# Kernel tuning notes

Hardware: AMD Instinct MI355X
Metric: run time of the kernel (lower is better)

The kernel has to match this reference:

```python
import jax, jax.numpy as jnp
import numpy as np

B, S, H, NH = 2, 2048, 1024, 16
HD = H // NH
ROTARY_DIM = 64
EPS = 1e-5
MINUS_INF = -10000.0


def _apply_rotary(q, k, rotary_dim):
    # q, k: [B, S, NH, HD]; GPT-NeoX style rotate_half on first rotary_dim dims
    pos = jnp.arange(S, dtype=jnp.float32)
    inv_freq = 1.0 / (10000.0 ** (jnp.arange(0, rotary_dim, 2, dtype=jnp.float32) / rotary_dim))
    freqs = pos[:, None] * inv_freq[None, :]                      # [S, rd/2]
    cos = jnp.concatenate([jnp.cos(freqs)] * 2, -1)[None, :, None, :]  # [1,S,1,rd]
    sin = jnp.concatenate([jnp.sin(freqs)] * 2, -1)[None, :, None, :]

    def rot(t):
        t_rot, t_pass = t[..., :rotary_dim], t[..., rotary_dim:]
        t1, t2 = jnp.split(t_rot, 2, axis=-1)
        rotated = jnp.concatenate([-t2, t1], axis=-1)
        return jnp.concatenate([t_rot * cos + rotated * sin, t_pass], axis=-1)

    return rot(q), rot(k)


def setup_inputs() -> dict:
    key = jax.random.key(0)
    ks = jax.random.split(key, 6)
    w_scale = 0.02
    return {
        "x": jax.random.normal(ks[0], (B, S, H), jnp.float32),
        "input_mask": jnp.ones((B, S), jnp.int32),
        "norm_w": jnp.ones((H,), jnp.float32),
        "norm_b": jnp.zeros((H,), jnp.float32),
        "attn_qkvw": jax.random.normal(ks[1], (H, 3 * H), jnp.float32) * w_scale,
        "attn_qkvb": jax.random.normal(ks[2], (3 * H,), jnp.float32) * w_scale,
        "attn_ow": jax.random.normal(ks[3], (H, H), jnp.float32) * w_scale,
        "attn_ob": jax.random.normal(ks[4], (H,), jnp.float32) * w_scale,
    }


def reference(x, input_mask, norm_w, norm_b, attn_qkvw, attn_qkvb, attn_ow, attn_ob):
    # pre-layernorm (qkv_gemm path with config.pre_layer_norm)
    mu = x.mean(-1, keepdims=True)
    var = x.var(-1, keepdims=True)
    xn = (x - mu) * jax.lax.rsqrt(var + EPS) * norm_w + norm_b

    # fused QKV projection
    qkv = xn @ attn_qkvw + attn_qkvb                       # [B,S,3H]
    q, k, v = jnp.split(qkv, 3, axis=-1)
    q = q.reshape(B, S, NH, HD)
    k = k.reshape(B, S, NH, HD)
    v = v.reshape(B, S, NH, HD)

    # rotary embedding on q,k
    q, k = _apply_rotary(q, k, ROTARY_DIM)

    # scaled scores + mask bias (1 - mask) * -10000 + triangular masking
    scale = 1.0 / np.sqrt(HD).astype(np.float32)
    scores = jnp.einsum("bqhd,bkhd->bhqk", q, k) * scale   # [B,NH,S,S]
    mask_bias = (1.0 - input_mask.astype(scores.dtype)) * MINUS_INF
    scores = scores + mask_bias[:, None, None, :]
    causal = jnp.tril(jnp.ones((S, S), bool))
    scores = jnp.where(causal[None, None], scores, MINUS_INF)

    probs = jax.nn.softmax(scores, axis=-1)
    ctx = jnp.einsum("bhqk,bkhd->bqhd", probs, v).reshape(B, S, H)

    # output projection (vector_matmul + bias)
    return ctx @ attn_ow + attn_ob
```

## Files before the change

kernel.cpp:

```cpp
#include <hip/hip_runtime.h>
#include <hip/hip_bf16.h>

#define B_  2
#define S_  2048
#define H_  1024
#define NH_ 16
#define HD_ 64
#define T_  (B_*S_)
#define H3_ (3*H_)

typedef float  floatx4 __attribute__((ext_vector_type(4)));
typedef __bf16 bf16x8  __attribute__((ext_vector_type(8)));

__device__ inline unsigned short f2bf_rn(float f) {
    union { float f; unsigned int u; } v; v.f = f;
    unsigned int u = v.u;
    u += 0x7fffu + ((u >> 16) & 1u);
    return (unsigned short)(u >> 16);
}
__device__ inline unsigned short f2bf_tr(float f) {
    union { float f; unsigned int u; } v; v.f = f;
    return (unsigned short)(v.u >> 16);
}
__device__ inline floatx4 fzero4() { floatx4 v; v[0]=0.f; v[1]=0.f; v[2]=0.f; v[3]=0.f; return v; }

__device__ inline void gload_lds16(const unsigned short* g, unsigned short* l) {
    __builtin_amdgcn_global_load_lds((const __attribute__((address_space(1))) unsigned int*)g,
                                     (__attribute__((address_space(3))) unsigned int*)l,
                                     16, 0, 0);
}

#define TLD 72
__global__ __launch_bounds__(256) void cvt_both_k(const float* __restrict__ qkvw,
                                                  const float* __restrict__ ow,
                                                  unsigned short* __restrict__ qkvwT,
                                                  unsigned short* __restrict__ owT) {
    __shared__ unsigned short Ts[64 * TLD];
    int id = blockIdx.x;
    const float* W; unsigned short* Wt; int N, nb, kb;
    if (id < 768) { W = qkvw; Wt = qkvwT; N = H3_; nb = (id % 48) * 64; kb = (id / 48) * 64; }
    else { id -= 768; W = ow; Wt = owT; N = H_; nb = (id % 16) * 64; kb = (id / 16) * 64; }
    const int K = H_;
    const int tid = threadIdx.x;
    #pragma unroll
    for (int p = 0; p < 4; p++) {
        const int krow = kb + p * 16 + (tid >> 4);
        const int ncol = (tid & 15) * 4;
        const float4 w = *reinterpret_cast<const float4*>(&W[(size_t)krow * N + nb + ncol]);
        Ts[(ncol + 0) * TLD + p * 16 + (tid >> 4)] = f2bf_rn(w.x);
        Ts[(ncol + 1) * TLD + p * 16 + (tid >> 4)] = f2bf_rn(w.y);
        Ts[(ncol + 2) * TLD + p * 16 + (tid >> 4)] = f2bf_rn(w.z);
        Ts[(ncol + 3) * TLD + p * 16 + (tid >> 4)] = f2bf_rn(w.w);
    }
    __syncthreads();
    #pragma unroll
    for (int p = 0; p < 2; p++) {
        const int n = (tid >> 3) + p * 32;
        const int k8 = (tid & 7) * 8;
        const uint4 v = *reinterpret_cast<const uint4*>(&Ts[n * TLD + k8]);
        *reinterpret_cast<uint4*>(&Wt[(size_t)(nb + n) * K + kb + k8]) = v;
    }
}

__global__ __launch_bounds__(256) void layernorm_k(const float* __restrict__ x,
                                                   const float* __restrict__ w,
                                                   const float* __restrict__ b,
                                                   unsigned short* __restrict__ xn) {
    const int t   = blockIdx.x;
    const int tid = threadIdx.x;
    const float4 v = reinterpret_cast<const float4*>(x + (size_t)t * H_)[tid];
    float s  = v.x + v.y + v.z + v.w;
    float s2 = v.x*v.x + v.y*v.y + v.z*v.z + v.w*v.w;
    for (int off = 32; off > 0; off >>= 1) {
        s  += __shfl_down(s,  off, 64);
        s2 += __shfl_down(s2, off, 64);
    }
    __shared__ float red[8];
    const int wave = tid >> 6, lane = tid & 63;
    if (lane == 0) { red[wave] = s; red[4 + wave] = s2; }
    __syncthreads();
    if (tid == 0) {
        red[0] = red[0] + red[1] + red[2] + red[3];
        red[4] = red[4] + red[5] + red[6] + red[7];
    }
    __syncthreads();
    const float mean = red[0] * (1.f / H_);
    const float var  = red[4] * (1.f / H_) - mean * mean;
    const float rstd = rsqrtf(var + 1e-5f);
    const float4 wv = reinterpret_cast<const float4*>(w)[tid];
    const float4 bv = reinterpret_cast<const float4*>(b)[tid];
    ushort4 o = make_ushort4(f2bf_rn((v.x - mean) * rstd * wv.x + bv.x),
                             f2bf_rn((v.y - mean) * rstd * wv.y + bv.y),
                             f2bf_rn((v.z - mean) * rstd * wv.z + bv.z),
                             f2bf_rn((v.w - mean) * rstd * wv.w + bv.w));
    reinterpret_cast<ushort4*>(xn + (size_t)t * H_)[tid] = o;
}

#define BM 128
#define BN 128

__device__ inline void gemm_core(const unsigned short* __restrict__ A,
                                 const unsigned short* __restrict__ Bt,
                                 int K, int mBase, int nBase,
                                 int tid, floatx4 acc[4][4],
                                 unsigned short* As0, unsigned short* As1,
                                 unsigned short* Bs0, unsigned short* Bs1) {
    const int lane = tid & 63;
    const int wave = tid >> 6;
    const int wr = wave >> 1, wc = wave & 1;
    const int srow = lane >> 2;
    const int scol = (lane & 3) * 8;
    const int mrow = lane & 15;
    const int koff = (lane >> 4) * 8;

    for (int kb = 0; kb < K; kb += 64) {
        __syncthreads();
        #pragma unroll
        for (int p = 0; p < 2; p++) {
            const int r = wave * 16 + p * 64;
            const size_t ga = (size_t)(mBase + r + srow) * K + kb + scol;
            const size_t gb = (size_t)(nBase + r + srow) * K + kb + scol;
            gload_lds16(&A [ga],      &As0[r * 32]);
            gload_lds16(&A [ga + 32], &As1[r * 32]);
            gload_lds16(&Bt[gb],      &Bs0[r * 32]);
            gload_lds16(&Bt[gb + 32], &Bs1[r * 32]);
        }
        __syncthreads();

        #pragma unroll
        for (int half = 0; half < 2; half++) {
            const unsigned short* As = half ? As1 : As0;
            const unsigned short* Bs = half ? Bs1 : Bs0;
            bf16x8 afrag[4], bfrag[4];
            #pragma unroll
            for (int mt = 0; mt < 4; mt++)
                afrag[mt] = *reinterpret_cast<const bf16x8*>(&As[(wr * 64 + mt * 16 + mrow) * 32 + koff]);
            #pragma unroll
            for (int nt = 0; nt < 4; nt++)
                bfrag[nt] = *reinterpret_cast<const bf16x8*>(&Bs[(wc * 64 + nt * 16 + mrow) * 32 + koff]);
            #pragma unroll
            for (int mt = 0; mt < 4; mt++)
                #pragma unroll
                for (int nt = 0; nt < 4; nt++)
                    acc[mt][nt] = __builtin_amdgcn_mfma_f32_16x16x32_bf16(afrag[mt], bfrag[nt], acc[mt][nt], 0, 0, 0);
        }
    }
}

__global__ __launch_bounds__(256) void gemm_qkv_k(const unsigned short* __restrict__ A,
                                                  const unsigned short* __restrict__ Bt,
                                                  const float* __restrict__ bias,
                                                  unsigned short* __restrict__ Qo,
                                                  unsigned short* __restrict__ Ko,
                                                  unsigned short* __restrict__ Vto) {
    __shared__ unsigned short As0[BM * 32], As1[BM * 32];
    __shared__ unsigned short Bs0[BN * 32], Bs1[BN * 32];

    const int tid  = threadIdx.x;
    const int lane = tid & 63;
    const int wave = tid >> 6;
    const int wr = wave >> 1, wc = wave & 1;
    const int mBase = blockIdx.y * BM;
    const int nBase = blockIdx.x * BN;

    floatx4 acc[4][4];
    #pragma unroll
    for (int i = 0; i < 4; i++)
        #pragma unroll
        for (int j = 0; j < 4; j++) acc[i][j] = fzero4();

    gemm_core(A, Bt, H_, mBase, nBase, tid, acc, As0, As1, Bs0, Bs1);

    const int col0 = lane & 15;
    const int r0   = (lane >> 4) * 4;
    const int hg   = (nBase + wc * 64) >> 6;
    const int sec  = hg >> 4;
    const int h    = hg & 15;

    float bs[4];
    #pragma unroll
    for (int nt = 0; nt < 4; nt++) bs[nt] = bias[nBase + wc * 64 + nt * 16 + col0];

    if (sec < 2) {
        unsigned short* dst = (sec == 0) ? Qo : Ko;
        const float if0 = __expf((float)col0        * (-0.2878231366f));
        const float if1 = __expf((float)(16 + col0) * (-0.2878231366f));
        #pragma unroll
        for (int mt = 0; mt < 4; mt++) {
            #pragma unroll
            for (int reg = 0; reg < 4; reg++) {
                const int t  = mBase + wr * 64 + mt * 16 + r0 + reg;
                const int bb = t >> 11;
                const int s  = t & (S_ - 1);
                float sn0, cs0, sn1, cs1;
                __sincosf((float)s * if0, &sn0, &cs0);
                __sincosf((float)s * if1, &sn1, &cs1);
                const float v0 = acc[mt][0][reg] + bs[0];
                const float v1 = acc[mt][1][reg] + bs[1];
                const float v2 = acc[mt][2][reg] + bs[2];
                const float v3 = acc[mt][3][reg] + bs[3];
                const float o0 = v0 * cs0 - v2 * sn0;
                const float o1 = v1 * cs1 - v3 * sn1;
                const float o2 = v2 * cs0 + v0 * sn0;
                const float o3 = v3 * cs1 + v1 * sn1;
                const size_t rb = ((size_t)(bb * NH_ + h) * S_ + s) * HD_;
                dst[rb +      col0] = f2bf_rn(o0);
                dst[rb + 16 + col0] = f2bf_rn(o1);
                dst[rb + 32 + col0] = f2bf_rn(o2);
                dst[rb + 48 + col0] = f2bf_rn(o3);
            }
        }
    } else {
        #pragma unroll
        for (int mt = 0; mt < 4; mt++) {
            const int t0 = mBase + wr * 64 + mt * 16 + r0;
            const int bb = t0 >> 11;
            const int s0 = t0 & (S_ - 1);
            #pragma unroll
            for (int nt = 0; nt < 4; nt++) {
                const int d = nt * 16 + col0;
                ushort4 o;
                o.x = f2bf_rn(acc[mt][nt][0] + bs[nt]);
                o.y = f2bf_rn(acc[mt][nt][1] + bs[nt]);
                o.z = f2bf_rn(acc[mt][nt][2] + bs[nt]);
                o.w = f2bf_rn(acc[mt][nt][3] + bs[nt]);
                *reinterpret_cast<ushort4*>(&Vto[((size_t)(bb * NH_ + h) * HD_ + d) * S_ + s0]) = o;
            }
        }
    }
}

__global__ __launch_bounds__(256) void gemm_proj_k(const unsigned short* __restrict__ A,
                                                   const unsigned short* __restrict__ Bt,
                                                   const float* __restrict__ bias,
                                                   float* __restrict__ Cf,
                                                   int M, int N, int K) {
    __shared__ unsigned short As0[BM * 32], As1[BM * 32];
    __shared__ unsigned short Bs0[BN * 32], Bs1[BN * 32];

    const int tid  = threadIdx.x;
    const int lane = tid & 63;
    const int wave = tid >> 6;
    const int wr = wave >> 1, wc = wave & 1;
    const int mBase = blockIdx.y * BM;
    const int nBase = blockIdx.x * BN;

    floatx4 acc[4][4];
    #pragma unroll
    for (int i = 0; i < 4; i++)
        #pragma unroll
        for (int j = 0; j < 4; j++) acc[i][j] = fzero4();

    gemm_core(A, Bt, K, mBase, nBase, tid, acc, As0, As1, Bs0, Bs1);

    const int col0 = lane & 15;
    const int r0   = (lane >> 4) * 4;
    #pragma unroll
    for (int mt = 0; mt < 4; mt++) {
        #pragma unroll
        for (int nt = 0; nt < 4; nt++) {
            const int gcol = nBase + wc * 64 + nt * 16 + col0;
            const float bsv = bias[gcol];
            #pragma unroll
            for (int reg = 0; reg < 4; reg++) {
                const int grow = mBase + wr * 64 + mt * 16 + r0 + reg;
                Cf[(size_t)grow * N + gcol] = acc[mt][nt][reg] + bsv;
            }
        }
    }
}

#define ALD 72
#define SCL2 0.1803368801f
#define MNEG -14427.0f

__global__ __launch_bounds__(256, 4) void attn_k(const unsigned short* __restrict__ Q,
                                                 const unsigned short* __restrict__ Kg,
                                                 const unsigned short* __restrict__ Vt,
                                                 const int* __restrict__ mask,
                                                 unsigned short* __restrict__ ctx) {
    const int id = blockIdx.x;
    const int bh = id & 31;
    const int v  = 31 - (id >> 5);
    const int b  = bh >> 4;
    const int h  = bh & 15;
    const int tid  = threadIdx.x;
    const int lane = tid & 63;
    const int wave = tid >> 6;

    __shared__ unsigned short Ks [64 * ALD];
    __shared__ unsigned short Vts[64 * ALD];
    __shared__ unsigned short Ps[4][16 * ALD];

    const size_t base = (size_t)bh * S_ * HD_;
    const int qbase = v * 64 + wave * 16;
    const int mrow = lane & 15;
    const int koff = (lane >> 4) * 8;
    const int r0   = (lane >> 4) * 4;
    const int col0 = lane & 15;

    bf16x8 qf0 = *reinterpret_cast<const bf16x8*>(&Q[base + (size_t)(qbase + mrow) * HD_ + koff]);
    bf16x8 qf1 = *reinterpret_cast<const bf16x8*>(&Q[base + (size_t)(qbase + mrow) * HD_ + 32 + koff]);

    bf16x8 onesf;
    {
        const __bf16 ov = (__bf16)((mrow == 0) ? 1.f : 0.f);
        #pragma unroll
        for (int q = 0; q < 8; q++) onesf[q] = ov;
    }

    floatx4 Oacc[4];
    floatx4 Lacc = fzero4();
    #pragma unroll
    for (int nt = 0; nt < 4; nt++) Oacc[nt] = fzero4();

    const int srow = tid >> 3;
    const int scol = (tid & 7) * 8;

    uint4 kreg0, kreg1, vreg0, vreg1;
    float mb0, mb1, mb2, mb3;
#define PREFETCH(KT) do {                                                                      \
        const int kb_ = (KT) * 64;                                                             \
        kreg0 = *reinterpret_cast<const uint4*>(&Kg[base + (size_t)(kb_ + srow)      * HD_ + scol]); \
        kreg1 = *reinterpret_cast<const uint4*>(&Kg[base + (size_t)(kb_ + srow + 32) * HD_ + scol]); \
        vreg0 = *reinterpret_cast<const uint4*>(&Vt[base + (size_t)srow        * S_ + kb_ + scol]);  \
        vreg1 = *reinterpret_cast<const uint4*>(&Vt[base + (size_t)(srow + 32) * S_ + kb_ + scol]);  \
        mb0 = (1.f - (float)mask[b * S_ + kb_ +  0 + col0]) * MNEG;                            \
        mb1 = (1.f - (float)mask[b * S_ + kb_ + 16 + col0]) * MNEG;                            \
        mb2 = (1.f - (float)mask[b * S_ + kb_ + 32 + col0]) * MNEG;                            \
        mb3 = (1.f - (float)mask[b * S_ + kb_ + 48 + col0]) * MNEG;                            \
    } while (0)

    PREFETCH(0);

    unsigned short* pw = Ps[wave];

    for (int kt = 0; kt <= v; kt++) {
        const int kb = kt * 64;
        if (kt) __syncthreads();
        *reinterpret_cast<uint4*>(&Ks [ srow       * ALD + scol]) = kreg0;
        *reinterpret_cast<uint4*>(&Ks [(srow + 32) * ALD + scol]) = kreg1;
        *reinterpret_cast<uint4*>(&Vts[ srow       * ALD + scol]) = vreg0;
        *reinterpret_cast<uint4*>(&Vts[(srow + 32) * ALD + scol]) = vreg1;
        __syncthreads();
        const float mc0 = mb0, mc1 = mb1, mc2 = mb2, mc3 = mb3;
        if (kt < v) PREFETCH(kt + 1);

        floatx4 sc[4];
        #pragma unroll
        for (int nt = 0; nt < 4; nt++) {
            const bf16x8 k0 = *reinterpret_cast<const bf16x8*>(&Ks[(nt * 16 + mrow) * ALD + koff]);
            const bf16x8 k1 = *reinterpret_cast<const bf16x8*>(&Ks[(nt * 16 + mrow) * ALD + 32 + koff]);
            floatx4 c = fzero4();
            c = __builtin_amdgcn_mfma_f32_16x16x32_bf16(qf0, k0, c, 0, 0, 0);
            c = __builtin_amdgcn_mfma_f32_16x16x32_bf16(qf1, k1, c, 0, 0, 0);
            sc[nt] = c;
        }
        #pragma unroll
        for (int nt = 0; nt < 4; nt++) {
            const float mbv = (nt == 0) ? mc0 : (nt == 1) ? mc1 : (nt == 2) ? mc2 : mc3;
            #pragma unroll
            for (int reg = 0; reg < 4; reg++)
                sc[nt][reg] = sc[nt][reg] * SCL2 + mbv;
        }
        if (kt == v) {
            #pragma unroll
            for (int nt = 0; nt < 4; nt++) {
                const int key = kb + nt * 16 + col0;
                #pragma unroll
                for (int reg = 0; reg < 4; reg++)
                    if (key > qbase + r0 + reg) sc[nt][reg] = MNEG;
            }
        }
        #pragma unroll
        for (int nt = 0; nt < 4; nt++)
            #pragma unroll
            for (int reg = 0; reg < 4; reg++)
                pw[(r0 + reg) * ALD + nt * 16 + col0] = f2bf_tr(exp2f(sc[nt][reg]));
        const bf16x8 p0 = *reinterpret_cast<const bf16x8*>(&pw[mrow * ALD + koff]);
        const bf16x8 p1 = *reinterpret_cast<const bf16x8*>(&pw[mrow * ALD + 32 + koff]);
        #pragma unroll
        for (int nt = 0; nt < 4; nt++) {
            const bf16x8 v0 = *reinterpret_cast<const bf16x8*>(&Vts[(nt * 16 + mrow) * ALD + koff]);
            const bf16x8 v1 = *reinterpret_cast<const bf16x8*>(&Vts[(nt * 16 + mrow) * ALD + 32 + koff]);
            Oacc[nt] = __builtin_amdgcn_mfma_f32_16x16x32_bf16(p0, v0, Oacc[nt], 0, 0, 0);
            Oacc[nt] = __builtin_amdgcn_mfma_f32_16x16x32_bf16(p1, v1, Oacc[nt], 0, 0, 0);
        }
        Lacc = __builtin_amdgcn_mfma_f32_16x16x32_bf16(p0, onesf, Lacc, 0, 0, 0);
        Lacc = __builtin_amdgcn_mfma_f32_16x16x32_bf16(p1, onesf, Lacc, 0, 0, 0);
    }
#undef PREFETCH

    float rl[4];
    #pragma unroll
    for (int reg = 0; reg < 4; reg++) {
        const float lsum = __shfl(Lacc[reg], lane & 48, 64);
        rl[reg] = 1.f / lsum;
    }
    #pragma unroll
    for (int nt = 0; nt < 4; nt++)
        #pragma unroll
        for (int reg = 0; reg < 4; reg++) {
            const int q = qbase + r0 + reg;
            const int d = nt * 16 + col0;
            ctx[((size_t)b * S_ + q) * H_ + h * HD_ + d] = f2bf_rn(Oacc[nt][reg] * rl[reg]);
        }
}

extern "C" void kernel_launch(void* const* d_in, const int* in_sizes, int n_in,
                              void* d_out, int out_size, void* d_ws, size_t ws_size,
                              hipStream_t stream) {
    const float* x     = (const float*)d_in[0];
    const int*   mask  = (const int*)d_in[1];
    const float* normw = (const float*)d_in[2];
    const float* normb = (const float*)d_in[3];
    const float* qkvw  = (const float*)d_in[4];
    const float* qkvb  = (const float*)d_in[5];
    const float* ow    = (const float*)d_in[6];
    const float* ob    = (const float*)d_in[7];
    float* out = (float*)d_out;

    char* ws = (char*)d_ws;
    unsigned short* xn_bf   = (unsigned short*)(ws);
    unsigned short* qkvwT   = (unsigned short*)(ws + (8ull  << 20));
    unsigned short* owT     = (unsigned short*)(ws + (14ull << 20));
    unsigned short* Qb      = (unsigned short*)(ws + (16ull << 20));
    unsigned short* Kb      = (unsigned short*)(ws + (24ull << 20));
    unsigned short* Vtb     = (unsigned short*)(ws + (32ull << 20));
    unsigned short* ctx_bf  = (unsigned short*)(ws + (40ull << 20));

    cvt_both_k<<<1024, 256, 0, stream>>>(qkvw, ow, qkvwT, owT);
    layernorm_k<<<T_, 256, 0, stream>>>(x, normw, normb, xn_bf);
    gemm_qkv_k<<<dim3(H3_ / BN, T_ / BM), 256, 0, stream>>>(xn_bf, qkvwT, qkvb, Qb, Kb, Vtb);
    attn_k<<<1024, 256, 0, stream>>>(Qb, Kb, Vtb, mask, ctx_bf);
    gemm_proj_k<<<dim3(H_ / BN, T_ / BM), 256, 0, stream>>>(ctx_bf, owT, ob, out, T_, H_, H_);
}
```

Measured before the change: 202.5 us.

## Process two key tiles per barrier in attention with doubled register prefetch

The attention loop now loads two 64-key K/V tiles into shared memory per iteration, prefetching both into registers and processing them back to back. This halves the number of block-wide barriers and gives longer stretches of MFMA work between global loads. In exchange it doubles the prefetch registers and the K/V shared memory, and lowers the launch-bounds occupancy hint from 4 to 3 blocks, which may reduce latency hiding. When the last pair is odd, the clamped second tile is loaded but skipped.

```diff
diff --git a/kernel.cpp b/kernel.cpp
--- a/kernel.cpp
+++ b/kernel.cpp
@@ -274,7 +274,7 @@
 #define SCL2 0.1803368801f
 #define MNEG -14427.0f
 
-__global__ __launch_bounds__(256, 4) void attn_k(const unsigned short* __restrict__ Q,
+__global__ __launch_bounds__(256, 3) void attn_k(const unsigned short* __restrict__ Q,
                                                  const unsigned short* __restrict__ Kg,
                                                  const unsigned short* __restrict__ Vt,
                                                  const int* __restrict__ mask,
@@ -288,8 +288,8 @@
     const int lane = tid & 63;
     const int wave = tid >> 6;
 
-    __shared__ unsigned short Ks [64 * ALD];
-    __shared__ unsigned short Vts[64 * ALD];
+    __shared__ unsigned short Ks [2][64 * ALD];
+    __shared__ unsigned short Vts[2][64 * ALD];
     __shared__ unsigned short Ps[4][16 * ALD];
 
     const size_t base = (size_t)bh * S_ * HD_;
@@ -317,79 +317,104 @@
     const int srow = tid >> 3;
     const int scol = (tid & 7) * 8;
 
-    uint4 kreg0, kreg1, vreg0, vreg1;
-    float mb0, mb1, mb2, mb3;
-#define PREFETCH(KT) do {                                                                      \
-        const int kb_ = (KT) * 64;                                                             \
-        kreg0 = *reinterpret_cast<const uint4*>(&Kg[base + (size_t)(kb_ + srow)      * HD_ + scol]); \
-        kreg1 = *reinterpret_cast<const uint4*>(&Kg[base + (size_t)(kb_ + srow + 32) * HD_ + scol]); \
-        vreg0 = *reinterpret_cast<const uint4*>(&Vt[base + (size_t)srow        * S_ + kb_ + scol]);  \
-        vreg1 = *reinterpret_cast<const uint4*>(&Vt[base + (size_t)(srow + 32) * S_ + kb_ + scol]);  \
-        mb0 = (1.f - (float)mask[b * S_ + kb_ +  0 + col0]) * MNEG;                            \
-        mb1 = (1.f - (float)mask[b * S_ + kb_ + 16 + col0]) * MNEG;                            \
-        mb2 = (1.f - (float)mask[b * S_ + kb_ + 32 + col0]) * MNEG;                            \
-        mb3 = (1.f - (float)mask[b * S_ + kb_ + 48 + col0]) * MNEG;                            \
+    uint4 k00, k01, k10, k11, v00, v01, v10, v11;
+    float mb00, mb01, mb02, mb03, mb10, mb11, mb12, mb13;
+#define PF_TILE(TT, KR0, KR1, VR0, VR1, M0, M1, M2, M3) do {                                   \
+        const int kb_ = (TT) * 64;                                                             \
+        KR0 = *reinterpret_cast<const uint4*>(&Kg[base + (size_t)(kb_ + srow)      * HD_ + scol]); \
+        KR1 = *reinterpret_cast<const uint4*>(&Kg[base + (size_t)(kb_ + srow + 32) * HD_ + scol]); \
+        VR0 = *reinterpret_cast<const uint4*>(&Vt[base + (size_t)srow        * S_ + kb_ + scol]);  \
+        VR1 = *reinterpret_cast<const uint4*>(&Vt[base + (size_t)(srow + 32) * S_ + kb_ + scol]);  \
+        M0 = (1.f - (float)mask[b * S_ + kb_ +  0 + col0]) * MNEG;                             \
+        M1 = (1.f - (float)mask[b * S_ + kb_ + 16 + col0]) * MNEG;                             \
+        M2 = (1.f - (float)mask[b * S_ + kb_ + 32 + col0]) * MNEG;                             \
+        M3 = (1.f - (float)mask[b * S_ + kb_ + 48 + col0]) * MNEG;                             \
     } while (0)
-
-    PREFETCH(0);
+#define PREFETCH_MACRO(MI) do {                                                                \
+        const int t0_ = min(2 * (MI), v);                                                      \
+        const int t1_ = min(2 * (MI) + 1, v);                                                  \
+        PF_TILE(t0_, k00, k01, v00, v01, mb00, mb01, mb02, mb03);                              \
+        PF_TILE(t1_, k10, k11, v10, v11, mb10, mb11, mb12, mb13);                              \
+    } while (0)
+
+    const int nmac = (v + 2) >> 1;
+    PREFETCH_MACRO(0);
 
     unsigned short* pw = Ps[wave];
 
-    for (int kt = 0; kt <= v; kt++) {
-        const int kb = kt * 64;
-        if (kt) __syncthreads();
-        *reinterpret_cast<uint4*>(&Ks [ srow       * ALD + scol]) = kreg0;
-        *reinterpret_cast<uint4*>(&Ks [(srow + 32) * ALD + scol]) = kreg1;
-        *reinterpret_cast<uint4*>(&Vts[ srow       * ALD + scol]) = vreg0;
-        *reinterpret_cast<uint4*>(&Vts[(srow + 32) * ALD + scol]) = vreg1;
+    for (int mi = 0; mi < nmac; mi++) {
+        if (mi) __syncthreads();
+        *reinterpret_cast<uint4*>(&Ks [0][ srow       * ALD + scol]) = k00;
+        *reinterpret_cast<uint4*>(&Ks [0][(srow + 32) * ALD + scol]) = k01;
+        *reinterpret_cast<uint4*>(&Ks [1][ srow       * ALD + scol]) = k10;
+        *reinterpret_cast<uint4*>(&Ks [1][(srow + 32) * ALD + scol]) = k11;
+        *reinterpret_cast<uint4*>(&Vts[0][ srow       * ALD + scol]) = v00;
+        *reinterpret_cast<uint4*>(&Vts[0][(srow + 32) * ALD + scol]) = v01;
+        *reinterpret_cast<uint4*>(&Vts[1][ srow       * ALD + scol]) = v10;
+        *reinterpret_cast<uint4*>(&Vts[1][(srow + 32) * ALD + scol]) = v11;
         __syncthreads();
-        const float mc0 = mb0, mc1 = mb1, mc2 = mb2, mc3 = mb3;
-        if (kt < v) PREFETCH(kt + 1);
-
-        floatx4 sc[4];
-        #pragma unroll
-        for (int nt = 0; nt < 4; nt++) {
-            const bf16x8 k0 = *reinterpret_cast<const bf16x8*>(&Ks[(nt * 16 + mrow) * ALD + koff]);
-            const bf16x8 k1 = *reinterpret_cast<const bf16x8*>(&Ks[(nt * 16 + mrow) * ALD + 32 + koff]);
-            floatx4 c = fzero4();
-            c = __builtin_amdgcn_mfma_f32_16x16x32_bf16(qf0, k0, c, 0, 0, 0);
-            c = __builtin_amdgcn_mfma_f32_16x16x32_bf16(qf1, k1, c, 0, 0, 0);
-            sc[nt] = c;
-        }
-        #pragma unroll
-        for (int nt = 0; nt < 4; nt++) {
-            const float mbv = (nt == 0) ? mc0 : (nt == 1) ? mc1 : (nt == 2) ? mc2 : mc3;
-            #pragma unroll
-            for (int reg = 0; reg < 4; reg++)
-                sc[nt][reg] = sc[nt][reg] * SCL2 + mbv;
-        }
-        if (kt == v) {
+        const float mc00 = mb00, mc01 = mb01, mc02 = mb02, mc03 = mb03;
+        const float mc10 = mb10, mc11 = mb11, mc12 = mb12, mc13 = mb13;
+        if (mi + 1 < nmac) PREFETCH_MACRO(mi + 1);
+
+        #pragma unroll
+        for (int half = 0; half < 2; half++) {
+            const int kt = 2 * mi + half;
+            if (half && kt > v) continue;
+            const int kb = kt * 64;
+            const unsigned short* ks = Ks [half];
+            const unsigned short* vs = Vts[half];
+            const float c0 = half ? mc10 : mc00;
+            const float c1 = half ? mc11 : mc01;
+            const float c2 = half ? mc12 : mc02;
+            const float c3 = half ? mc13 : mc03;
+
+            floatx4 sc[4];
             #pragma unroll
             for (int nt = 0; nt < 4; nt++) {
-                const int key = kb + nt * 16 + col0;
+                const bf16x8 kf0 = *reinterpret_cast<const bf16x8*>(&ks[(nt * 16 + mrow) * ALD + koff]);
+                const bf16x8 kf1 = *reinterpret_cast<const bf16x8*>(&ks[(nt * 16 + mrow) * ALD + 32 + koff]);
+                floatx4 c = fzero4();
+                c = __builtin_amdgcn_mfma_f32_16x16x32_bf16(qf0, kf0, c, 0, 0, 0);
+                c = __builtin_amdgcn_mfma_f32_16x16x32_bf16(qf1, kf1, c, 0, 0, 0);
+                sc[nt] = c;
+            }
+            #pragma unroll
+            for (int nt = 0; nt < 4; nt++) {
+                const float mbv = (nt == 0) ? c0 : (nt == 1) ? c1 : (nt == 2) ? c2 : c3;
                 #pragma unroll
                 for (int reg = 0; reg < 4; reg++)
-                    if (key > qbase + r0 + reg) sc[nt][reg] = MNEG;
-            }
-        }
-        #pragma unroll
-        for (int nt = 0; nt < 4; nt++)
-            #pragma unroll
-            for (int reg = 0; reg < 4; reg++)
-                pw[(r0 + reg) * ALD + nt * 16 + col0] = f2bf_tr(exp2f(sc[nt][reg]));
-        const bf16x8 p0 = *reinterpret_cast<const bf16x8*>(&pw[mrow * ALD + koff]);
-        const bf16x8 p1 = *reinterpret_cast<const bf16x8*>(&pw[mrow * ALD + 32 + koff]);
-        #pragma unroll
-        for (int nt = 0; nt < 4; nt++) {
-            const bf16x8 v0 = *reinterpret_cast<const bf16x8*>(&Vts[(nt * 16 + mrow) * ALD + koff]);
-            const bf16x8 v1 = *reinterpret_cast<const bf16x8*>(&Vts[(nt * 16 + mrow) * ALD + 32 + koff]);
-            Oacc[nt] = __builtin_amdgcn_mfma_f32_16x16x32_bf16(p0, v0, Oacc[nt], 0, 0, 0);
-            Oacc[nt] = __builtin_amdgcn_mfma_f32_16x16x32_bf16(p1, v1, Oacc[nt], 0, 0, 0);
-        }
-        Lacc = __builtin_amdgcn_mfma_f32_16x16x32_bf16(p0, onesf, Lacc, 0, 0, 0);
-        Lacc = __builtin_amdgcn_mfma_f32_16x16x32_bf16(p1, onesf, Lacc, 0, 0, 0);
-    }
-#undef PREFETCH
+                    sc[nt][reg] = sc[nt][reg] * SCL2 + mbv;
+            }
+            if (kt == v) {
+                #pragma unroll
+                for (int nt = 0; nt < 4; nt++) {
+                    const int key = kb + nt * 16 + col0;
+                    #pragma unroll
+                    for (int reg = 0; reg < 4; reg++)
+                        if (key > qbase + r0 + reg) sc[nt][reg] = MNEG;
+                }
+            }
+            #pragma unroll
+            for (int nt = 0; nt < 4; nt++)
+                #pragma unroll
+                for (int reg = 0; reg < 4; reg++)
+                    pw[(r0 + reg) * ALD + nt * 16 + col0] = f2bf_tr(exp2f(sc[nt][reg]));
+            const bf16x8 p0 = *reinterpret_cast<const bf16x8*>(&pw[mrow * ALD + koff]);
+            const bf16x8 p1 = *reinterpret_cast<const bf16x8*>(&pw[mrow * ALD + 32 + koff]);
+            #pragma unroll
+            for (int nt = 0; nt < 4; nt++) {
+                const bf16x8 vf0 = *reinterpret_cast<const bf16x8*>(&vs[(nt * 16 + mrow) * ALD + koff]);
+                const bf16x8 vf1 = *reinterpret_cast<const bf16x8*>(&vs[(nt * 16 + mrow) * ALD + 32 + koff]);
+                Oacc[nt] = __builtin_amdgcn_mfma_f32_16x16x32_bf16(p0, vf0, Oacc[nt], 0, 0, 0);
+                Oacc[nt] = __builtin_amdgcn_mfma_f32_16x16x32_bf16(p1, vf1, Oacc[nt], 0, 0, 0);
+            }
+            Lacc = __builtin_amdgcn_mfma_f32_16x16x32_bf16(p0, onesf, Lacc, 0, 0, 0);
+            Lacc = __builtin_amdgcn_mfma_f32_16x16x32_bf16(p1, onesf, Lacc, 0, 0, 0);
+        }
+    }
+#undef PREFETCH_MACRO
+#undef PF_TILE
 
     float rl[4];
     #pragma unroll
```

Result: no change. 199.1 us (-1.7%).
